# Kernel tuning notes

Hardware: AMD Instinct MI355X
Metric: run time of the kernel (lower is better)

## Reference

```python
import jax, jax.numpy as jnp
import numpy as np

B, N, A = 4096, 16, 8          # envs, num_agents, num_actions
D_IN, H1, DP, DZ = 128, 64, 64, 64  # obs dim, gnn hidden, obs_proc dim, gat fc dim


def _init(k, shape):
    return jax.random.normal(k, shape, jnp.float32) / np.sqrt(shape[0]).astype(np.float32)


def setup_inputs() -> dict:
    key = jax.random.key(0)
    ks = jax.random.split(key, 8)
    return {
        "obs": jax.random.normal(ks[0], (B * N, D_IN), jnp.float32),
        "policies": jax.random.uniform(ks[1], (B * N, A), dtype=jnp.float32),
        "actions": jax.random.uniform(ks[2], (B * N, A), dtype=jnp.float32),
        "W1": _init(ks[3], (D_IN, H1)), "b1": jnp.zeros((H1,), jnp.float32),
        "W2": _init(ks[4], (H1, DP)), "b2": jnp.zeros((DP,), jnp.float32),
        "Wfc": _init(ks[5], (DP, DZ)),
        "Wattn": _init(ks[6], (2 * DZ, 1)),
        "Wv": _init(ks[7], (DP + A, 1)), "bv": jnp.zeros((1,), jnp.float32),
    }


def reference(obs, policies, actions, W1, b1, W2, b2, Wfc, Wattn, Wv, bv):
    obs = obs.reshape(B, N, D_IN)
    # --- CriticInputPreprocess: two mean-aggregation GNN layers on a complete
    # graph with self-loops -> every node sees the per-env mean.
    agg1 = jnp.mean(obs, axis=1)                      # [B, D_IN]
    h = jax.nn.relu(agg1 @ W1 + b1)                   # [B, H1] (identical across nodes)
    obs_proc1 = h @ W2 + b2                           # mean of identical features is itself
    obs_proc = jnp.broadcast_to(obs_proc1[:, None, :], (B, N, DP))  # [B, N, DP]
    # --- GATLayer edge attention: e_{d<-s} = leaky_relu(attn([z_s, z_d]))
    z_ = obs_proc @ Wfc                               # [B, N, DZ]
    a_src = (z_ @ Wattn[:DZ]).squeeze(-1)             # [B, N]
    a_dst = (z_ @ Wattn[DZ:]).squeeze(-1)             # [B, N]
    e = jax.nn.leaky_relu(a_src[:, None, :] + a_dst[:, :, None])    # [B, dst, src]
    w = jax.nn.sigmoid(e)                             # [B, N, N]
    pi = policies.reshape(B, N, A)
    act = actions.reshape(B, N, A)
    # mailbox mix per (dst d, src k): z = w*act_k + (1-w)*pi_k
    z = w[..., None] * act[:, None, :, :] + (1.0 - w[..., None]) * pi[:, None, :, :]  # [B,d,k,A]
    # place_policies/place_zs + mean over src axis collapses to:
    # y[b,d,j] = (pi[b,j] + sum_{k!=j} z[b,d,k]) / N
    y = (jnp.sum(z, axis=2, keepdims=True) - z + pi[:, None, :, :]) / N               # [B,d,j,A]
    obs_rep = jnp.broadcast_to(obs_proc[:, None, :, :], (B, N, N, DP))                # obs_proc[b, j]
    obs_final = jnp.concatenate([obs_rep, y], axis=-1).reshape(B * N, N, DP + A)
    x = obs_final @ Wv + bv                           # [B*N, N, 1]
    return x, w.reshape(B * N, N, 1)
```

## Files before the change

kernel.cpp:

```cpp
#include <hip/hip_runtime.h>

#define BB   4096
#define NN   16
#define AA   8
#define DIN  128
#define H1C  64
#define DPC  64
#define DZC  64

#define GENV 8
#define NTHR 512
#define LDT  132

__global__ __launch_bounds__(NTHR, 4)
void critic_kernel(const float* __restrict__ obs,
                   const float* __restrict__ policies,
                   const float* __restrict__ actions,
                   const float* __restrict__ W1,
                   const float* __restrict__ b1,
                   const float* __restrict__ W2,
                   const float* __restrict__ b2,
                   const float* __restrict__ Wfc,
                   const float* __restrict__ Wattn,
                   const float* __restrict__ Wv,
                   const float* __restrict__ bv,
                   float* __restrict__ out_x,
                   float* __restrict__ out_w)
{
    __shared__ float sW1T[H1C][LDT];
    __shared__ float sAgg[GENV][DIN];
    __shared__ float sV1[H1C];
    __shared__ float sV2[H1C];
    __shared__ float sS[2];
    __shared__ float sDv[GENV][16];
    __shared__ float sWsum[DZC];
    __shared__ float sWv64[DPC];
    __shared__ float sU[DPC];

    const int tid = threadIdx.x;
    const int l   = tid & 63;
    const int w   = tid >> 6;
    const int e   = blockIdx.x * GENV + w;

    const float2* o2p = reinterpret_cast<const float2*>(obs) + (size_t)e * (NN * DIN / 2);
    float2 ov[NN];
    #pragma unroll
    for (int r = 0; r < NN; ++r) ov[r] = o2p[r * 64 + l];

    {
        const float4* g1 = reinterpret_cast<const float4*>(W1);
        #pragma unroll
        for (int i = 0; i < (DIN * H1C / 4) / NTHR; ++i) {
            const int g = i * NTHR + tid;
            const float4 v = g1[g];
            const int d  = g >> 4;
            const int c4 = (g & 15) * 4;
            sW1T[c4 + 0][d] = v.x;
            sW1T[c4 + 1][d] = v.y;
            sW1T[c4 + 2][d] = v.z;
            sW1T[c4 + 3][d] = v.w;
        }
    }

    const float* Pb = policies + (size_t)e * (NN * AA);
    const float* Ab = actions  + (size_t)e * (NN * AA);
    const float pv0 = Pb[l], pv1 = Pb[64 + l];
    const float av0 = Ab[l], av1 = Ab[64 + l];

    const float b1v = b1[l];
    const float va  = Wv[64 + (l & 7)];
    const float bvv = bv[0];

    if (w == 7) {
        const float b2v  = b2[l];
        const float wsum = Wattn[l] + Wattn[DZC + l];
        const float wvv  = Wv[l];
        sWsum[l] = wsum;
        sWv64[l] = wvv;

        float u = 0.0f;
        {
            const float4* WfcR = reinterpret_cast<const float4*>(Wfc) + (size_t)l * (DZC / 4);
            const float4* ws4  = reinterpret_cast<const float4*>(sWsum);
            #pragma unroll
            for (int j4 = 0; j4 < DZC / 4; ++j4) {
                const float4 wq = WfcR[j4];
                const float4 s  = ws4[j4];
                u = fmaf(wq.x, s.x, u); u = fmaf(wq.y, s.y, u);
                u = fmaf(wq.z, s.z, u); u = fmaf(wq.w, s.w, u);
            }
        }
        sU[l] = u;
        float v1 = 0.0f, v2 = 0.0f;
        {
            const float4* W2R = reinterpret_cast<const float4*>(W2) + (size_t)l * (DPC / 4);
            const float4* su4 = reinterpret_cast<const float4*>(sU);
            const float4* sv4 = reinterpret_cast<const float4*>(sWv64);
            #pragma unroll
            for (int j4 = 0; j4 < DPC / 4; ++j4) {
                const float4 wq = W2R[j4];
                const float4 a  = su4[j4];
                const float4 b  = sv4[j4];
                v1 = fmaf(wq.x, a.x, v1); v1 = fmaf(wq.y, a.y, v1);
                v1 = fmaf(wq.z, a.z, v1); v1 = fmaf(wq.w, a.w, v1);
                v2 = fmaf(wq.x, b.x, v2); v2 = fmaf(wq.y, b.y, v2);
                v2 = fmaf(wq.z, b.z, v2); v2 = fmaf(wq.w, b.w, v2);
            }
        }
        float tb2u = b2v * u;
        float tb2w = b2v * wvv;
        #pragma unroll
        for (int m = 32; m >= 1; m >>= 1) {
            tb2u += __shfl_xor(tb2u, m);
            tb2w += __shfl_xor(tb2w, m);
        }
        sV1[l] = v1;
        sV2[l] = v2;
        if (l == 0) { sS[0] = tb2u; sS[1] = tb2w; }
    }

    {
        float sx = 0.0f, sy = 0.0f;
        #pragma unroll
        for (int r = 0; r < NN; ++r) { sx += ov[r].x; sy += ov[r].y; }
        const float inv = 1.0f / 16.0f;
        *reinterpret_cast<float2*>(&sAgg[w][2 * l]) = make_float2(sx * inv, sy * inv);
    }

    __syncthreads();

    float a0 = b1v, a1 = 0.0f, a2 = 0.0f, a3 = 0.0f;
    #pragma unroll
    for (int d4 = 0; d4 < DIN / 4; ++d4) {
        const float4 w4 = *reinterpret_cast<const float4*>(&sW1T[l][4 * d4]);
        const float4 ag = *reinterpret_cast<const float4*>(&sAgg[w][4 * d4]);
        a0 = fmaf(ag.x, w4.x, a0);
        a1 = fmaf(ag.y, w4.y, a1);
        a2 = fmaf(ag.z, w4.z, a2);
        a3 = fmaf(ag.w, w4.w, a3);
    }
    const float h = fmaxf((a0 + a1) + (a2 + a3), 0.0f);

    const float v1l  = sV1[l];
    const float v2l  = sV2[l];
    const float tb2u = sS[0];
    const float tb2w = sS[1];

    float t0 = h * v1l;
    float t1 = h * v2l;
    #pragma unroll
    for (int m = 32; m >= 1; m >>= 1) {
        t0 += __shfl_xor(t0, m);
        t1 += __shfl_xor(t1, m);
    }
    const float logit = t0 + tb2u;
    const float eV  = (logit > 0.0f) ? logit : 0.01f * logit;
    const float wgt = 1.0f / (1.0f + expf(-eV));
    const float c   = t1 + tb2w + bvv;

    float q0 = (pv0 - av0) * va;
    float q1 = (pv1 - av1) * va;
    float fq = q0 + q1;
    float fp = (pv0 + pv1) * va;
    #pragma unroll
    for (int m = 1; m <= 4; m <<= 1) {
        q0 += __shfl_xor(q0, m);
        q1 += __shfl_xor(q1, m);
    }
    #pragma unroll
    for (int m = 32; m >= 1; m >>= 1) {
        fq += __shfl_xor(fq, m);
        fp += __shfl_xor(fp, m);
    }
    const float Sv = fp - wgt * fq;

    if ((l & 7) == 0) {
        sDv[w][l >> 3]       = q0;
        sDv[w][8 + (l >> 3)] = q1;
    }

    const float invN = 1.0f / 16.0f;
    const int j0 = (4 * l) & 15;
    float4 xo, wo;
    xo.x = fmaf(wgt, sDv[w][j0 + 0], Sv) * invN + c;
    xo.y = fmaf(wgt, sDv[w][j0 + 1], Sv) * invN + c;
    xo.z = fmaf(wgt, sDv[w][j0 + 2], Sv) * invN + c;
    xo.w = fmaf(wgt, sDv[w][j0 + 3], Sv) * invN + c;
    wo.x = wo.y = wo.z = wo.w = wgt;

    const size_t base = (size_t)e * (NN * NN) + 4 * l;
    *reinterpret_cast<float4*>(out_x + base) = xo;
    *reinterpret_cast<float4*>(out_w + base) = wo;
}

extern "C" void kernel_launch(void* const* d_in, const int* in_sizes, int n_in,
                              void* d_out, int out_size, void* d_ws, size_t ws_size,
                              hipStream_t stream) {
    const float* obs      = (const float*)d_in[0];
    const float* policies = (const float*)d_in[1];
    const float* actions  = (const float*)d_in[2];
    const float* W1       = (const float*)d_in[3];
    const float* b1       = (const float*)d_in[4];
    const float* W2       = (const float*)d_in[5];
    const float* b2       = (const float*)d_in[6];
    const float* Wfc      = (const float*)d_in[7];
    const float* Wattn    = (const float*)d_in[8];
    const float* Wv       = (const float*)d_in[9];
    const float* bv       = (const float*)d_in[10];

    float* out_x = (float*)d_out;
    float* out_w = out_x + (size_t)BB * NN * NN;

    critic_kernel<<<BB / GENV, NTHR, 0, stream>>>(obs, policies, actions,
                                                  W1, b1, W2, b2, Wfc, Wattn, Wv, bv,
                                                  out_x, out_w);
}
```

Baseline: 17.80 us.

## Swizzle W1 transpose in LDS, broadcast aggregates via readlane, hoist policy reductions

```diff
diff --git a/kernel.cpp b/kernel.cpp
--- a/kernel.cpp
+++ b/kernel.cpp
@@ -10,7 +10,11 @@
 
 #define GENV 8
 #define NTHR 512
-#define LDT  132
+
+
+__device__ __forceinline__ float lane_bcast(float v, int lane) {
+    return __int_as_float(__builtin_amdgcn_readlane(__float_as_int(v), lane));
+}
 
 __global__ __launch_bounds__(NTHR, 4)
 void critic_kernel(const float* __restrict__ obs,
@@ -27,8 +31,7 @@
                    float* __restrict__ out_x,
                    float* __restrict__ out_w)
 {
-    __shared__ float sW1T[H1C][LDT];
-    __shared__ float sAgg[GENV][DIN];
+    __shared__ float4 sW1T4[H1C * 32];
     __shared__ float sV1[H1C];
     __shared__ float sV2[H1C];
     __shared__ float sS[2];
@@ -42,25 +45,24 @@
     const int w   = tid >> 6;
     const int e   = blockIdx.x * GENV + w;
 
+    {
+        const int c   = tid & 63;
+        const int grp = tid >> 6;
+        #pragma unroll
+        for (int i = 0; i < 4; ++i) {
+            const int d0 = 4 * (i * 8 + grp);
+            const float w0  = W1[(d0 + 0) * H1C + c];
+            const float w1_ = W1[(d0 + 1) * H1C + c];
+            const float w2_ = W1[(d0 + 2) * H1C + c];
+            const float w3_ = W1[(d0 + 3) * H1C + c];
+            sW1T4[c * 32 + ((d0 >> 2) ^ (c & 7))] = make_float4(w0, w1_, w2_, w3_);
+        }
+    }
+
     const float2* o2p = reinterpret_cast<const float2*>(obs) + (size_t)e * (NN * DIN / 2);
     float2 ov[NN];
     #pragma unroll
     for (int r = 0; r < NN; ++r) ov[r] = o2p[r * 64 + l];
-
-    {
-        const float4* g1 = reinterpret_cast<const float4*>(W1);
-        #pragma unroll
-        for (int i = 0; i < (DIN * H1C / 4) / NTHR; ++i) {
-            const int g = i * NTHR + tid;
-            const float4 v = g1[g];
-            const int d  = g >> 4;
-            const int c4 = (g & 15) * 4;
-            sW1T[c4 + 0][d] = v.x;
-            sW1T[c4 + 1][d] = v.y;
-            sW1T[c4 + 2][d] = v.z;
-            sW1T[c4 + 3][d] = v.w;
-        }
-    }
 
     const float* Pb = policies + (size_t)e * (NN * AA);
     const float* Ab = actions  + (size_t)e * (NN * AA);
@@ -119,12 +121,33 @@
         if (l == 0) { sS[0] = tb2u; sS[1] = tb2w; }
     }
 
+    float ax, ay;
     {
         float sx = 0.0f, sy = 0.0f;
         #pragma unroll
         for (int r = 0; r < NN; ++r) { sx += ov[r].x; sy += ov[r].y; }
         const float inv = 1.0f / 16.0f;
-        *reinterpret_cast<float2*>(&sAgg[w][2 * l]) = make_float2(sx * inv, sy * inv);
+        ax = sx * inv;
+        ay = sy * inv;
+    }
+
+    float q0 = (pv0 - av0) * va;
+    float q1 = (pv1 - av1) * va;
+    float fq = q0 + q1;
+    float fp = (pv0 + pv1) * va;
+    #pragma unroll
+    for (int m = 1; m <= 4; m <<= 1) {
+        q0 += __shfl_xor(q0, m);
+        q1 += __shfl_xor(q1, m);
+    }
+    #pragma unroll
+    for (int m = 32; m >= 1; m >>= 1) {
+        fq += __shfl_xor(fq, m);
+        fp += __shfl_xor(fp, m);
+    }
+    if ((l & 7) == 0) {
+        sDv[w][l >> 3]       = q0;
+        sDv[w][8 + (l >> 3)] = q1;
     }
 
     __syncthreads();
@@ -132,12 +155,11 @@
     float a0 = b1v, a1 = 0.0f, a2 = 0.0f, a3 = 0.0f;
     #pragma unroll
     for (int d4 = 0; d4 < DIN / 4; ++d4) {
-        const float4 w4 = *reinterpret_cast<const float4*>(&sW1T[l][4 * d4]);
-        const float4 ag = *reinterpret_cast<const float4*>(&sAgg[w][4 * d4]);
-        a0 = fmaf(ag.x, w4.x, a0);
-        a1 = fmaf(ag.y, w4.y, a1);
-        a2 = fmaf(ag.z, w4.z, a2);
-        a3 = fmaf(ag.w, w4.w, a3);
+        const float4 w4 = sW1T4[l * 32 + (d4 ^ (l & 7))];
+        a0 = fmaf(lane_bcast(ax, 2 * d4),     w4.x, a0);
+        a1 = fmaf(lane_bcast(ay, 2 * d4),     w4.y, a1);
+        a2 = fmaf(lane_bcast(ax, 2 * d4 + 1), w4.z, a2);
+        a3 = fmaf(lane_bcast(ay, 2 * d4 + 1), w4.w, a3);
     }
     const float h = fmaxf((a0 + a1) + (a2 + a3), 0.0f);
 
@@ -157,27 +179,7 @@
     const float eV  = (logit > 0.0f) ? logit : 0.01f * logit;
     const float wgt = 1.0f / (1.0f + expf(-eV));
     const float c   = t1 + tb2w + bvv;
-
-    float q0 = (pv0 - av0) * va;
-    float q1 = (pv1 - av1) * va;
-    float fq = q0 + q1;
-    float fp = (pv0 + pv1) * va;
-    #pragma unroll
-    for (int m = 1; m <= 4; m <<= 1) {
-        q0 += __shfl_xor(q0, m);
-        q1 += __shfl_xor(q1, m);
-    }
-    #pragma unroll
-    for (int m = 32; m >= 1; m >>= 1) {
-        fq += __shfl_xor(fq, m);
-        fp += __shfl_xor(fp, m);
-    }
-    const float Sv = fp - wgt * fq;
-
-    if ((l & 7) == 0) {
-        sDv[w][l >> 3]       = q0;
-        sDv[w][8 + (l >> 3)] = q1;
-    }
+    const float Sv  = fp - wgt * fq;
 
     const float invN = 1.0f / 16.0f;
     const int j0 = (4 * l) & 15;
```

Measured after the change: 17.42 us. -2.1%, faster.
